# Kernel tuning notes

Measured on AMD Instinct MI355X. Metric: run time of the kernel, lower is better.

The kernel has to match this reference:

```python
import jax, jax.numpy as jnp
import numpy as np

N = 200000   # lane-graph nodes
C = 128      # n_map
S = 6        # num_scales
EP = 100000  # edges per pre/suc scale
EL = 25000   # left/right edges
EPS = 1e-5


def gn1(x, g, b):
    # GroupNorm(1, C) over shape [N, C]: normalize per node across channels, affine per channel
    mu = jnp.mean(x, axis=-1, keepdims=True)
    var = jnp.mean(jnp.square(x - mu), axis=-1, keepdims=True)
    return (x - mu) * jax.lax.rsqrt(var + EPS) * g + b


def setup_inputs() -> dict:
    key = jax.random.key(0)
    ks = jax.random.split(key, 32)
    f = lambda i, shape, s=1.0: jax.random.normal(ks[i], shape, dtype=jnp.float32) * s
    sc = 1.0 / np.sqrt(C)
    inp = {
        'control':   f(0, (N,)),
        'turn':      f(1, (N, 2)),
        'intersect': f(2, (N,)),
        'ctrs':      f(3, (N, 2)),
        'feats':     f(4, (N, 2)),
        'pre':   jax.random.randint(ks[5], (S, 2, EP), 0, N, dtype=jnp.int32),
        'suc':   jax.random.randint(ks[6], (S, 2, EP), 0, N, dtype=jnp.int32),
        'left':  jax.random.randint(ks[7], (2, EL), 0, N, dtype=jnp.int32),
        'right': jax.random.randint(ks[8], (2, EL), 0, N, dtype=jnp.int32),
        # input branch: Linear(2,C)+b, ReLU, Linear(C,C,no bias)+GroupNorm(1,C)
        'w_in1': f(9, (2, C), 0.7), 'b_in1': jnp.zeros((C,), jnp.float32),
        'w_in2': f(10, (C, C), sc), 'gn_in_g': jnp.ones((C,), jnp.float32), 'gn_in_b': jnp.zeros((C,), jnp.float32),
        # seg branch
        'w_seg1': f(11, (2, C), 0.7), 'b_seg1': jnp.zeros((C,), jnp.float32),
        'w_seg2': f(12, (C, C), sc), 'gn_seg_g': jnp.ones((C,), jnp.float32), 'gn_seg_b': jnp.zeros((C,), jnp.float32),
        # meta: Linear(C+4,C,no bias)+GN+ReLU
        'w_meta': f(13, (C + 4, C), sc), 'gn_meta_g': jnp.ones((C,), jnp.float32), 'gn_meta_b': jnp.zeros((C,), jnp.float32),
        # fuse dict, 4 layers
        'ctr_w':   f(14, (4, C, C), sc),
        'pre_w':   f(15, (4, S, C, C), sc),
        'suc_w':   f(16, (4, S, C, C), sc),
        'left_w':  f(17, (4, C, C), sc),
        'right_w': f(18, (4, C, C), sc),
        'norm_g': jnp.ones((4, C), jnp.float32), 'norm_b': jnp.zeros((4, C), jnp.float32),
        'ctr2_w': f(19, (4, C, C), sc),
        'ctr2_g': jnp.ones((4, C), jnp.float32), 'ctr2_b': jnp.zeros((4, C), jnp.float32),
    }
    return inp


def reference(control, turn, intersect, ctrs, feats, pre, suc, left, right,
              w_in1, b_in1, w_in2, gn_in_g, gn_in_b,
              w_seg1, b_seg1, w_seg2, gn_seg_g, gn_seg_b,
              w_meta, gn_meta_g, gn_meta_b,
              ctr_w, pre_w, suc_w, left_w, right_w,
              norm_g, norm_b, ctr2_w, ctr2_g, ctr2_b):
    # input / seg branches
    a = gn1(jax.nn.relu(ctrs @ w_in1 + b_in1) @ w_in2, gn_in_g, gn_in_b)
    b = gn1(jax.nn.relu(feats @ w_seg1 + b_seg1) @ w_seg2, gn_seg_g, gn_seg_b)
    feat = jax.nn.relu(a + b)
    # meta fuse
    meta = jnp.concatenate([feat, turn, control[:, None], intersect[:, None]], axis=1)
    feat = jax.nn.relu(gn1(meta @ w_meta, gn_meta_g, gn_meta_b))
    res = feat
    for i in range(4):
        temp = feat @ ctr_w[i]
        # multi-scale pre/suc: gather -> per-scale linear -> scatter-add
        pre_msg = jnp.einsum('sec,scd->sed', feat[pre[:, 1]], pre_w[i])   # [S,EP,C]
        temp = temp.at[pre[:, 0].reshape(-1)].add(pre_msg.reshape(-1, C))
        suc_msg = jnp.einsum('sec,scd->sed', feat[suc[:, 1]], suc_w[i])
        temp = temp.at[suc[:, 0].reshape(-1)].add(suc_msg.reshape(-1, C))
        temp = temp.at[left[0]].add(feat[left[1]] @ left_w[i])
        temp = temp.at[right[0]].add(feat[right[1]] @ right_w[i])
        feat = jax.nn.relu(gn1(temp, norm_g[i], norm_b[i]))
        feat = gn1(feat @ ctr2_w[i], ctr2_g[i], ctr2_b[i])
        feat = jax.nn.relu(feat + res)
        res = feat
    return (feat, ctrs)
```

## Files before the change

### kernel.cpp

```cpp
#include <hip/hip_runtime.h>

#define N_NODES 200000
#define CDIM 128
#define NSCALE 6
#define NEP 100000
#define NEL 25000
#define NCLS 14
#define NCHUNK 196

typedef unsigned short u16;
typedef unsigned int u32;

using fragAB = __attribute__((ext_vector_type(8))) short;
using fragC  = __attribute__((ext_vector_type(4))) float;

enum { P_PLAIN = 0, P_TWO = 1, P_META = 2 };
enum { E_GN = 1, E_RELU = 2 };

__device__ __forceinline__ float4 ld4(const float* p) { return *(const float4*)p; }

__device__ __forceinline__ u16 f2bf(float f) {
  u32 u = __builtin_bit_cast(u32, f);
  u = (u + 0x7fff + ((u >> 16) & 1)) >> 16;
  return (u16)u;
}
__device__ __forceinline__ u32 pk2(float a, float b) {
  return (u32)f2bf(a) | ((u32)f2bf(b) << 16);
}
__device__ __forceinline__ float bflo(u32 u) { return __builtin_bit_cast(float, u << 16); }
__device__ __forceinline__ float bfhi(u32 u) { return __builtin_bit_cast(float, u & 0xffff0000u); }

__device__ __forceinline__ void acc16(float* s, uint4 a, uint4 b) {
  s[0] += bflo(a.x); s[1] += bfhi(a.x); s[2]  += bflo(a.y); s[3]  += bfhi(a.y);
  s[4] += bflo(a.z); s[5] += bfhi(a.z); s[6]  += bflo(a.w); s[7]  += bfhi(a.w);
  s[8] += bflo(b.x); s[9] += bfhi(b.x); s[10] += bflo(b.y); s[11] += bfhi(b.y);
  s[12] += bflo(b.z); s[13] += bfhi(b.z); s[14] += bflo(b.w); s[15] += bfhi(b.w);
}

__host__ __device__ constexpr int idx_base(int c) {
  return (c < 12) ? c * NEP : 12 * NEP + (c - 12) * NEL;
}

__device__ __forceinline__ int wslot(int li, int c) {
  if (c < 0)  return 2 + li;
  if (c < 6)  return 18 + li * 6 + c;
  if (c < 12) return 42 + li * 6 + (c - 6);
  return (c == 12) ? (10 + li) : (14 + li);
}

template<int PRO, int EPI>
__global__ __launch_bounds__(256)
void mm_k(int M, int Kp,
          const float* __restrict__ Af, const float* __restrict__ A2f,
          const float* __restrict__ e0, const float* __restrict__ e1, const float* __restrict__ e2,
          const u16* __restrict__ Wt,
          float* __restrict__ Y, u16* __restrict__ Yb,
          const float* __restrict__ gn_g, const float* __restrict__ gn_b)
{
  constexpr int LSTR = 56;
  __shared__ u16 As[128 * LSTR];
  __shared__ u16 Bs[128 * LSTR];

  const int tid = threadIdx.x;
  const int lane = tid & 63, wid = tid >> 6;
  const int wm = (wid >> 1) * 64, wn = (wid & 1) * 64;
  const int q = lane >> 4, l16 = lane & 15;
  const int row0 = blockIdx.x * 128;
  const int srow = tid >> 1, shalf = tid & 1;

  fragC acc[4][4];
  #pragma unroll
  for (int i = 0; i < 4; i++)
    #pragma unroll
    for (int j = 0; j < 4; j++)
      #pragma unroll
      for (int e = 0; e < 4; e++) acc[i][j][e] = 0.0f;

  const int sgrow = row0 + srow;
  const bool svalid = (sgrow < M);
  float x0 = 0.f, x1 = 0.f, mx = 0.f, my = 0.f, mc = 0.f, mi = 0.f;
  if constexpr (PRO == P_TWO) {
    if (svalid) { x0 = Af[(size_t)sgrow * 2]; x1 = Af[(size_t)sgrow * 2 + 1]; }
  }
  if constexpr (PRO == P_META) {
    if (svalid) { mx = e0[(size_t)sgrow * 2]; my = e0[(size_t)sgrow * 2 + 1]; mc = e1[sgrow]; mi = e2[sgrow]; }
  }

  const int nk = Kp >> 5;
  for (int kt = 0; kt < nk; ++kt) {
    const int k0 = kt * 32 + shalf * 16;
    {
      u16* adst = &As[srow * LSTR + shalf * 16];
      float v[16];
      #pragma unroll
      for (int j = 0; j < 16; j++) v[j] = 0.f;
      if constexpr (PRO == P_TWO) {
        #pragma unroll
        for (int j0 = 0; j0 < 16; j0 += 4) {
          float4 wa = ld4(e0 + k0 + j0);
          float4 wb = ld4(e0 + 128 + k0 + j0);
          float4 bb = ld4(e1 + k0 + j0);
          v[j0]     = fmaxf(0.f, fmaf(x0, wa.x, fmaf(x1, wb.x, bb.x)));
          v[j0 + 1] = fmaxf(0.f, fmaf(x0, wa.y, fmaf(x1, wb.y, bb.y)));
          v[j0 + 2] = fmaxf(0.f, fmaf(x0, wa.z, fmaf(x1, wb.z, bb.z)));
          v[j0 + 3] = fmaxf(0.f, fmaf(x0, wa.w, fmaf(x1, wb.w, bb.w)));
        }
      } else {
        if (svalid) {
          if (k0 < 128) {
            const float* sa = Af + (size_t)sgrow * 128 + k0;
            const float* sb = A2f + (size_t)sgrow * 128 + k0;
            #pragma unroll
            for (int j0 = 0; j0 < 16; j0 += 4) {
              float4 a = ld4(sa + j0), b = ld4(sb + j0);
              v[j0]     = fmaxf(0.f, a.x + b.x);
              v[j0 + 1] = fmaxf(0.f, a.y + b.y);
              v[j0 + 2] = fmaxf(0.f, a.z + b.z);
              v[j0 + 3] = fmaxf(0.f, a.w + b.w);
            }
          } else {
            #pragma unroll
            for (int j = 0; j < 16; j++) {
              const int kk = k0 + j - 128;
              v[j] = (kk == 0) ? mx : (kk == 1) ? my : (kk == 2) ? mc : (kk == 3) ? mi : 0.f;
            }
          }
        }
      }
      u32 p[8];
      #pragma unroll
      for (int j = 0; j < 8; j++) p[j] = pk2(v[2 * j], v[2 * j + 1]);
      *(uint4*)adst = make_uint4(p[0], p[1], p[2], p[3]);
      *(uint4*)(adst + 8) = make_uint4(p[4], p[5], p[6], p[7]);
    }
    {
      const u16* s = Wt + (size_t)srow * Kp + k0;
      uint4 b0 = *(const uint4*)s, b1 = *(const uint4*)(s + 8);
      u16* bdst = &Bs[srow * LSTR + shalf * 16];
      *(uint4*)bdst = b0; *(uint4*)(bdst + 8) = b1;
    }
    __syncthreads();
    fragAB af[4], bf[4];
    #pragma unroll
    for (int t = 0; t < 4; t++) af[t] = *(const fragAB*)&As[(wm + t * 16 + l16) * LSTR + q * 8];
    #pragma unroll
    for (int t = 0; t < 4; t++) bf[t] = *(const fragAB*)&Bs[(wn + t * 16 + l16) * LSTR + q * 8];
    #pragma unroll
    for (int mt = 0; mt < 4; mt++)
      #pragma unroll
      for (int nt = 0; nt < 4; nt++)
        acc[mt][nt] = __builtin_amdgcn_mfma_f32_16x16x32_bf16(af[mt], bf[nt], acc[mt][nt], 0, 0, 0);
    __syncthreads();
  }

  __shared__ float2 red[128][2];
  __shared__ float2 stats[128];
  #pragma unroll
  for (int mt = 0; mt < 4; mt++)
    #pragma unroll
    for (int r = 0; r < 4; r++) {
      float s1 = acc[mt][0][r] + acc[mt][1][r] + acc[mt][2][r] + acc[mt][3][r];
      float s2 = acc[mt][0][r] * acc[mt][0][r] + acc[mt][1][r] * acc[mt][1][r]
               + acc[mt][2][r] * acc[mt][2][r] + acc[mt][3][r] * acc[mt][3][r];
      #pragma unroll
      for (int off = 1; off < 16; off <<= 1) {
        s1 += __shfl_xor(s1, off, 64);
        s2 += __shfl_xor(s2, off, 64);
      }
      if (l16 == 0) red[wm + mt * 16 + q * 4 + r][wid & 1] = make_float2(s1, s2);
    }
  __syncthreads();
  if (tid < 128) {
    const float2 p0 = red[tid][0], p1 = red[tid][1];
    const float m = (p0.x + p1.x) * (1.0f / 128.0f);
    const float var = (p0.y + p1.y) * (1.0f / 128.0f) - m * m;
    stats[tid] = make_float2(m, rsqrtf(var + 1e-5f));
  }
  __syncthreads();
  float gl[4], bl[4];
  #pragma unroll
  for (int nt = 0; nt < 4; nt++) {
    gl[nt] = gn_g[wn + nt * 16 + l16];
    bl[nt] = gn_b[wn + nt * 16 + l16];
  }
  #pragma unroll
  for (int mt = 0; mt < 4; mt++)
    #pragma unroll
    for (int r = 0; r < 4; r++) {
      const int rl = wm + mt * 16 + q * 4 + r;
      const int grow = row0 + rl;
      if (grow >= M) continue;
      const float2 st = stats[rl];
      #pragma unroll
      for (int nt = 0; nt < 4; nt++) {
        const int col = wn + nt * 16 + l16;
        float v = (acc[mt][nt][r] - st.x) * st.y * gl[nt] + bl[nt];
        if constexpr ((EPI & E_RELU) != 0) v = fmaxf(v, 0.f);
        if (Y)  Y[(size_t)grow * 128 + col] = v;
        if (Yb) Yb[(size_t)grow * 128 + col] = f2bf(v);
      }
    }
}

__global__ __launch_bounds__(256, 3)
void layer_k(const u16* __restrict__ Fin, u16* __restrict__ Fout,
             float* __restrict__ outf,
             const int* __restrict__ ptrs, const int* __restrict__ idxs,
             const u16* __restrict__ Wt, int li,
             const float* __restrict__ g1, const float* __restrict__ b1,
             const float* __restrict__ g2, const float* __restrict__ b2)
{
  constexpr int LSTR = 56, FSTR = 136;
  __shared__ u16 ldsA[128 * FSTR];
  __shared__ u16 Bs[128 * LSTR];
  __shared__ float2 red[128][2];
  __shared__ float2 stats[128];

  const int tid = threadIdx.x;
  const int lane = tid & 63, wid = tid >> 6;
  const int wm = (wid >> 1) * 64, wn = (wid & 1) * 64;
  const int q = lane >> 4, l16 = lane & 15;
  const int row0 = blockIdx.x * 128;
  const int srow = tid >> 1, shalf = tid & 1;
  const int sgrow = row0 + srow;
  const bool svalid = (sgrow < N_NODES);

  fragC acc[4][4];
  #pragma unroll
  for (int i = 0; i < 4; i++)
    #pragma unroll
    for (int j = 0; j < 4; j++)
      #pragma unroll
      for (int e = 0; e < 4; e++) acc[i][j][e] = 0.0f;

  for (int c = -1; c < NCLS; ++c) {
    const u16* W = Wt + (size_t)wslot(li, c) * 16384;

    if (c < 0) {
      uint4 a[8];
      #pragma unroll
      for (int j = 0; j < 8; j++) a[j] = make_uint4(0, 0, 0, 0);
      if (svalid) {
        const u16* s = Fin + (size_t)sgrow * 128 + shalf * 64;
        #pragma unroll
        for (int j = 0; j < 8; j++) a[j] = ((const uint4*)s)[j];
      }
      u16* adst = &ldsA[srow * FSTR + shalf * 64];
      #pragma unroll
      for (int j = 0; j < 8; j++) ((uint4*)adst)[j] = a[j];
    } else {
      int lo = 0, hi = 0;
      if (svalid) {
        const int* pc = ptrs + (size_t)c * (N_NODES + 1);
        hi = pc[sgrow]; lo = sgrow ? pc[sgrow - 1] : 0;
      }
      const int* ic = idxs + idx_base(c);
      #pragma unroll 1
      for (int hf = 0; hf < 2; ++hf) {
        const int off = shalf * 64 + hf * 32;
        float s[32];
        #pragma unroll
        for (int j = 0; j < 32; j++) s[j] = 0.f;
        int p = lo;
        for (; p + 2 <= hi; p += 2) {
          const u16* sp0 = Fin + (size_t)ic[p] * 128 + off;
          const u16* sp1 = Fin + (size_t)ic[p + 1] * 128 + off;
          uint4 a0 = ((const uint4*)sp0)[0], a1 = ((const uint4*)sp0)[1];
          uint4 a2 = ((const uint4*)sp0)[2], a3 = ((const uint4*)sp0)[3];
          uint4 b0 = ((const uint4*)sp1)[0], b1 = ((const uint4*)sp1)[1];
          uint4 b2 = ((const uint4*)sp1)[2], b3 = ((const uint4*)sp1)[3];
          acc16(s, a0, a1); acc16(s + 16, a2, a3);
          acc16(s, b0, b1); acc16(s + 16, b2, b3);
        }
        if (p < hi) {
          const u16* sp = Fin + (size_t)ic[p] * 128 + off;
          acc16(s, ((const uint4*)sp)[0], ((const uint4*)sp)[1]);
          acc16(s + 16, ((const uint4*)sp)[2], ((const uint4*)sp)[3]);
        }
        u32 pk[16];
        #pragma unroll
        for (int j = 0; j < 16; j++) pk[j] = pk2(s[2 * j], s[2 * j + 1]);
        u16* adst = &ldsA[srow * FSTR + off];
        ((uint4*)adst)[0] = make_uint4(pk[0],  pk[1],  pk[2],  pk[3]);
        ((uint4*)adst)[1] = make_uint4(pk[4],  pk[5],  pk[6],  pk[7]);
        ((uint4*)adst)[2] = make_uint4(pk[8],  pk[9],  pk[10], pk[11]);
        ((uint4*)adst)[3] = make_uint4(pk[12], pk[13], pk[14], pk[15]);
      }
    }

    uint4 pb0, pb1;
    {
      const u16* ws = W + (size_t)srow * 128 + shalf * 16;
      pb0 = *(const uint4*)ws; pb1 = *(const uint4*)(ws + 8);
    }
    __syncthreads();

    #pragma unroll
    for (int kt = 0; kt < 4; ++kt) {
      u16* bdst = &Bs[srow * LSTR + shalf * 16];
      *(uint4*)bdst = pb0; *(uint4*)(bdst + 8) = pb1;
      if (kt < 3) {
        const u16* ws = W + (size_t)srow * 128 + (kt + 1) * 32 + shalf * 16;
        pb0 = *(const uint4*)ws; pb1 = *(const uint4*)(ws + 8);
      }
      __syncthreads();
      fragAB af[4], bf[4];
      #pragma unroll
      for (int t = 0; t < 4; t++) af[t] = *(const fragAB*)&ldsA[(wm + t * 16 + l16) * FSTR + kt * 32 + q * 8];
      #pragma unroll
      for (int t = 0; t < 4; t++) bf[t] = *(const fragAB*)&Bs[(wn + t * 16 + l16) * LSTR + q * 8];
      #pragma unroll
      for (int mt = 0; mt < 4; mt++)
        #pragma unroll
        for (int nt = 0; nt < 4; nt++)
          acc[mt][nt] = __builtin_amdgcn_mfma_f32_16x16x32_bf16(af[mt], bf[nt], acc[mt][nt], 0, 0, 0);
      __syncthreads();
    }
  }

  #pragma unroll
  for (int mt = 0; mt < 4; mt++)
    #pragma unroll
    for (int r = 0; r < 4; r++) {
      float s1 = acc[mt][0][r] + acc[mt][1][r] + acc[mt][2][r] + acc[mt][3][r];
      float s2 = acc[mt][0][r] * acc[mt][0][r] + acc[mt][1][r] * acc[mt][1][r]
               + acc[mt][2][r] * acc[mt][2][r] + acc[mt][3][r] * acc[mt][3][r];
      #pragma unroll
      for (int off = 1; off < 16; off <<= 1) {
        s1 += __shfl_xor(s1, off, 64);
        s2 += __shfl_xor(s2, off, 64);
      }
      if (l16 == 0) red[wm + mt * 16 + q * 4 + r][wid & 1] = make_float2(s1, s2);
    }
  __syncthreads();
  if (tid < 128) {
    const float2 p0 = red[tid][0], p1 = red[tid][1];
    const float m = (p0.x + p1.x) * (1.0f / 128.0f);
    const float var = (p0.y + p1.y) * (1.0f / 128.0f) - m * m;
    stats[tid] = make_float2(m, rsqrtf(var + 1e-5f));
  }
  __syncthreads();
  {
    float gl[4], bl[4];
    #pragma unroll
    for (int nt = 0; nt < 4; nt++) {
      gl[nt] = g1[wn + nt * 16 + l16];
      bl[nt] = b1[wn + nt * 16 + l16];
    }
    #pragma unroll
    for (int mt = 0; mt < 4; mt++)
      #pragma unroll
      for (int r = 0; r < 4; r++) {
        const int rl = wm + mt * 16 + q * 4 + r;
        const float2 st = stats[rl];
        #pragma unroll
        for (int nt = 0; nt < 4; nt++) {
          const int col = wn + nt * 16 + l16;
          const float v = fmaxf(0.f, (acc[mt][nt][r] - st.x) * st.y * gl[nt] + bl[nt]);
          ldsA[rl * FSTR + col] = f2bf(v);
        }
      }
  }

  #pragma unroll
  for (int i = 0; i < 4; i++)
    #pragma unroll
    for (int j = 0; j < 4; j++)
      #pragma unroll
      for (int e = 0; e < 4; e++) acc[i][j][e] = 0.0f;
  {
    const u16* W2 = Wt + (size_t)(6 + li) * 16384;
    #pragma unroll
    for (int kt = 0; kt < 4; ++kt) {
      const int k0 = kt * 32 + shalf * 16;
      const u16* ws = W2 + (size_t)srow * 128 + k0;
      uint4 a = *(const uint4*)ws, b = *(const uint4*)(ws + 8);
      u16* bdst = &Bs[srow * LSTR + shalf * 16];
      *(uint4*)bdst = a; *(uint4*)(bdst + 8) = b;
      __syncthreads();
      fragAB af[4], bf[4];
      #pragma unroll
      for (int t = 0; t < 4; t++) af[t] = *(const fragAB*)&ldsA[(wm + t * 16 + l16) * FSTR + kt * 32 + q * 8];
      #pragma unroll
      for (int t = 0; t < 4; t++) bf[t] = *(const fragAB*)&Bs[(wn + t * 16 + l16) * LSTR + q * 8];
      #pragma unroll
      for (int mt = 0; mt < 4; mt++)
        #pragma unroll
        for (int nt = 0; nt < 4; nt++)
          acc[mt][nt] = __builtin_amdgcn_mfma_f32_16x16x32_bf16(af[mt], bf[nt], acc[mt][nt], 0, 0, 0);
      __syncthreads();
    }
  }

  #pragma unroll
  for (int mt = 0; mt < 4; mt++)
    #pragma unroll
    for (int r = 0; r < 4; r++) {
      float s1 = acc[mt][0][r] + acc[mt][1][r] + acc[mt][2][r] + acc[mt][3][r];
      float s2 = acc[mt][0][r] * acc[mt][0][r] + acc[mt][1][r] * acc[mt][1][r]
               + acc[mt][2][r] * acc[mt][2][r] + acc[mt][3][r] * acc[mt][3][r];
      #pragma unroll
      for (int off = 1; off < 16; off <<= 1) {
        s1 += __shfl_xor(s1, off, 64);
        s2 += __shfl_xor(s2, off, 64);
      }
      if (l16 == 0) red[wm + mt * 16 + q * 4 + r][wid & 1] = make_float2(s1, s2);
    }
  __syncthreads();
  if (tid < 128) {
    const float2 p0 = red[tid][0], p1 = red[tid][1];
    const float m = (p0.x + p1.x) * (1.0f / 128.0f);
    const float var = (p0.y + p1.y) * (1.0f / 128.0f) - m * m;
    stats[tid] = make_float2(m, rsqrtf(var + 1e-5f));
  }
  __syncthreads();
  {
    float gl[4], bl[4];
    #pragma unroll
    for (int nt = 0; nt < 4; nt++) {
      gl[nt] = g2[wn + nt * 16 + l16];
      bl[nt] = b2[wn + nt * 16 + l16];
    }
    #pragma unroll
    for (int mt = 0; mt < 4; mt++)
      #pragma unroll
      for (int r = 0; r < 4; r++) {
        const int rl = wm + mt * 16 + q * 4 + r;
        const int grow = row0 + rl;
        if (grow >= N_NODES) continue;
        const float2 st = stats[rl];
        #pragma unroll
        for (int nt = 0; nt < 4; nt++) {
          const int col = wn + nt * 16 + l16;
          const float res = bflo((u32)Fin[(size_t)grow * 128 + col]);
          float v = (acc[mt][nt][r] - st.x) * st.y * gl[nt] + bl[nt] + res;
          v = fmaxf(v, 0.f);
          if (outf) outf[(size_t)grow * 128 + col] = v;
          else      Fout[(size_t)grow * 128 + col] = f2bf(v);
        }
      }
  }
}

__global__ __launch_bounds__(256)
void prep_k(const float* __restrict__ in2, const float* __restrict__ seg2,
            const float* __restrict__ ctr, const float* __restrict__ ctr2,
            const float* __restrict__ lw, const float* __restrict__ rw,
            const float* __restrict__ pw, const float* __restrict__ sw,
            const float* __restrict__ meta, u16* __restrict__ Wt)
{
  const int id = blockIdx.x;
  const float* src;
  int K = 128, Kp = 128;
  if (id == 0) src = in2;
  else if (id == 1) src = seg2;
  else if (id < 6)  src = ctr  + (size_t)(id - 2) * 16384;
  else if (id < 10) src = ctr2 + (size_t)(id - 6) * 16384;
  else if (id < 14) src = lw   + (size_t)(id - 10) * 16384;
  else if (id < 18) src = rw   + (size_t)(id - 14) * 16384;
  else if (id < 42) src = pw   + (size_t)(id - 18) * 16384;
  else if (id < 66) src = sw   + (size_t)(id - 42) * 16384;
  else { src = meta; K = 132; Kp = 160; }
  u16* dst = Wt + (size_t)id * 16384;
  const int tot = 128 * Kp;
  for (int e = threadIdx.x; e < tot; e += 256) {
    const int n = e & 127, k = e >> 7;
    const float v = (k < K) ? src[(size_t)k * 128 + n] : 0.f;
    dst[(size_t)n * Kp + k] = f2bf(v);
  }
}

struct EdgeCfg { const int* dst[NCLS]; const int* src[NCLS]; int cnt[NCLS]; };

__global__ __launch_bounds__(256)
void hist_k(EdgeCfg cfg, int* __restrict__ ptrs)
{
  const int c = blockIdx.y;
  const int i = blockIdx.x * 256 + threadIdx.x;
  if (i < cfg.cnt[c]) atomicAdd(ptrs + (size_t)c * (N_NODES + 1) + cfg.dst[c][i], 1);
}

__global__ __launch_bounds__(256)
void scan1_k(const int* __restrict__ ptrs, int* __restrict__ part)
{
  const int c = blockIdx.y, b = blockIdx.x;
  const int* d = ptrs + (size_t)c * (N_NODES + 1) + b * 1024;
  const int rem = min(1024, N_NODES - b * 1024);
  int s = 0;
  for (int j = threadIdx.x; j < rem; j += 256) s += d[j];
  #pragma unroll
  for (int off = 32; off; off >>= 1) s += __shfl_xor(s, off, 64);
  __shared__ int r[4];
  if ((threadIdx.x & 63) == 0) r[threadIdx.x >> 6] = s;
  __syncthreads();
  if (threadIdx.x == 0) part[c * NCHUNK + b] = r[0] + r[1] + r[2] + r[3];
}

__global__ __launch_bounds__(64)
void scan2_k(int* __restrict__ part, int* __restrict__ ptrs)
{
  const int c = blockIdx.x;
  if (threadIdx.x) return;
  int* p = part + c * NCHUNK;
  int run = 0;
  for (int b = 0; b < NCHUNK; b++) { const int t = p[b]; p[b] = run; run += t; }
  ptrs[(size_t)c * (N_NODES + 1) + N_NODES] = run;
}

__global__ __launch_bounds__(256)
void scan3_k(int* __restrict__ ptrs, const int* __restrict__ part)
{
  const int c = blockIdx.y, b = blockIdx.x;
  int* d = ptrs + (size_t)c * (N_NODES + 1) + b * 1024;
  const int base = part[c * NCHUNK + b];
  const int gbase = b * 1024;
  const int i0 = threadIdx.x * 4;
  int v[4];
  #pragma unroll
  for (int j = 0; j < 4; j++) v[j] = (gbase + i0 + j < N_NODES) ? d[i0 + j] : 0;
  const int tsum = v[0] + v[1] + v[2] + v[3];
  __shared__ int sc[256];
  sc[threadIdx.x] = tsum;
  __syncthreads();
  #pragma unroll
  for (int off = 1; off < 256; off <<= 1) {
    const int t = (threadIdx.x >= off) ? sc[threadIdx.x - off] : 0;
    __syncthreads();
    sc[threadIdx.x] += t;
    __syncthreads();
  }
  int run = sc[threadIdx.x] - tsum + base;
  #pragma unroll
  for (int j = 0; j < 4; j++) {
    if (gbase + i0 + j < N_NODES) d[i0 + j] = run;
    run += v[j];
  }
}

__global__ __launch_bounds__(256)
void fill_k(EdgeCfg cfg, int* __restrict__ ptrs, int* __restrict__ idxs)
{
  const int c = blockIdx.y;
  const int i = blockIdx.x * 256 + threadIdx.x;
  if (i >= cfg.cnt[c]) return;
  const int d = cfg.dst[c][i];
  const int slot = atomicAdd(ptrs + (size_t)c * (N_NODES + 1) + d, 1);
  idxs[idx_base(c) + slot] = cfg.src[c][i];
}

__global__ __launch_bounds__(256)
void copy_k(const float* __restrict__ src, float* __restrict__ dst, int n)
{
  const int i = blockIdx.x * 256 + threadIdx.x;
  if (i < n) dst[i] = src[i];
}

extern "C" void kernel_launch(void* const* d_in, const int* in_sizes, int n_in,
                              void* d_out, int out_size, void* d_ws, size_t ws_size,
                              hipStream_t stream) {
  const float* control   = (const float*)d_in[0];
  const float* turn      = (const float*)d_in[1];
  const float* intersect = (const float*)d_in[2];
  const float* ctrs      = (const float*)d_in[3];
  const float* feats     = (const float*)d_in[4];
  const int*   pre   = (const int*)d_in[5];
  const int*   suc   = (const int*)d_in[6];
  const int*   left  = (const int*)d_in[7];
  const int*   right = (const int*)d_in[8];
  const float* w_in1   = (const float*)d_in[9];
  const float* b_in1   = (const float*)d_in[10];
  const float* w_in2   = (const float*)d_in[11];
  const float* gn_in_g = (const float*)d_in[12];
  const float* gn_in_b = (const float*)d_in[13];
  const float* w_seg1   = (const float*)d_in[14];
  const float* b_seg1   = (const float*)d_in[15];
  const float* w_seg2   = (const float*)d_in[16];
  const float* gn_seg_g = (const float*)d_in[17];
  const float* gn_seg_b = (const float*)d_in[18];
  const float* w_meta    = (const float*)d_in[19];
  const float* gn_meta_g = (const float*)d_in[20];
  const float* gn_meta_b = (const float*)d_in[21];
  const float* ctr_w   = (const float*)d_in[22];
  const float* pre_w   = (const float*)d_in[23];
  const float* suc_w   = (const float*)d_in[24];
  const float* left_w  = (const float*)d_in[25];
  const float* right_w = (const float*)d_in[26];
  const float* norm_g  = (const float*)d_in[27];
  const float* norm_b  = (const float*)d_in[28];
  const float* ctr2_w  = (const float*)d_in[29];
  const float* ctr2_g  = (const float*)d_in[30];
  const float* ctr2_b  = (const float*)d_in[31];

  const size_t NF = (size_t)N_NODES * CDIM;
  char* w = (char*)d_ws;
  float* Ta = (float*)w;  w += NF * 4;
  float* Tb = (float*)w;  w += NF * 4;
  u16* Fb0  = (u16*)w;    w += NF * 2;
  u16* Fb1  = (u16*)w;    w += NF * 2;
  u16* Wt   = (u16*)w;    w += (size_t)(67 * 16384 + 128 * 160) * 2;
  int* ptrs = (int*)w;    w += (size_t)NCLS * (N_NODES + 1) * 4;
  int* idxs = (int*)w;    w += (size_t)(12 * NEP + 2 * NEL) * 4;
  int* part = (int*)w;
  float* out = (float*)d_out;

  EdgeCfg cfg;
  for (int s = 0; s < NSCALE; s++) {
    cfg.dst[s] = pre + (size_t)s * 2 * NEP;     cfg.src[s] = pre + ((size_t)s * 2 + 1) * NEP;     cfg.cnt[s] = NEP;
    cfg.dst[6 + s] = suc + (size_t)s * 2 * NEP; cfg.src[6 + s] = suc + ((size_t)s * 2 + 1) * NEP; cfg.cnt[6 + s] = NEP;
  }
  cfg.dst[12] = left;  cfg.src[12] = left + NEL;  cfg.cnt[12] = NEL;
  cfg.dst[13] = right; cfg.src[13] = right + NEL; cfg.cnt[13] = NEL;

  const dim3 blk(256);
  const dim3 gN((N_NODES + 127) / 128);
  const dim3 gHist((NEP + 255) / 256, NCLS);
  const dim3 gScan(NCHUNK, NCLS);

  prep_k<<<dim3(67), blk, 0, stream>>>(w_in2, w_seg2, ctr_w, ctr2_w, left_w, right_w,
                                       pre_w, suc_w, w_meta, Wt);
  (void)hipMemsetAsync(ptrs, 0, (size_t)NCLS * (N_NODES + 1) * sizeof(int), stream);
  hist_k<<<gHist, blk, 0, stream>>>(cfg, ptrs);
  scan1_k<<<gScan, blk, 0, stream>>>(ptrs, part);
  scan2_k<<<dim3(NCLS), dim3(64), 0, stream>>>(part, ptrs);
  scan3_k<<<gScan, blk, 0, stream>>>(ptrs, part);
  fill_k<<<gHist, blk, 0, stream>>>(cfg, ptrs, idxs);

  mm_k<P_TWO, E_GN><<<gN, blk, 0, stream>>>(N_NODES, 128, ctrs, nullptr,
      w_in1, b_in1, nullptr, Wt + 0 * 16384, Ta, nullptr, gn_in_g, gn_in_b);
  mm_k<P_TWO, E_GN><<<gN, blk, 0, stream>>>(N_NODES, 128, feats, nullptr,
      w_seg1, b_seg1, nullptr, Wt + 1 * 16384, Tb, nullptr, gn_seg_g, gn_seg_b);
  mm_k<P_META, E_GN | E_RELU><<<gN, blk, 0, stream>>>(N_NODES, 160, Ta, Tb,
      turn, control, intersect, Wt + 66 * 16384, nullptr, Fb0, gn_meta_g, gn_meta_b);

  for (int i = 0; i < 4; i++) {
    const u16* Fin = (i & 1) ? Fb1 : Fb0;
    u16* Fout      = (i & 1) ? Fb0 : Fb1;
    layer_k<<<gN, blk, 0, stream>>>(Fin, Fout, (i == 3) ? out : nullptr,
        ptrs, idxs, Wt, i,
        norm_g + i * 128, norm_b + i * 128, ctr2_g + i * 128, ctr2_b + i * 128);
  }

  copy_k<<<dim3((2 * N_NODES + 255) / 256), blk, 0, stream>>>(ctrs, out + NF, 2 * N_NODES);
}
```

Before: 2.068 ms.

## Load MFMA weight fragments directly from global, drop B staging in LDS

Removes the shared-memory B tile: weight fragments for every GEMM are now read straight from global (L2-resident) memory into MFMA registers. The first ctr GEMM also reads the A operand directly from Fin instead of staging it in LDS. This cuts LDS use and most per-k-tile barriers, and raises launch bounds to 4 blocks per CU. It also drops the 2-way unroll of the gather loop. The cost is more global or L2 load traffic and latency on the MFMA inner loop, plus tighter register pressure.

```diff
diff --git a/kernel.cpp b/kernel.cpp
--- a/kernel.cpp
+++ b/kernel.cpp
@@ -202,7 +202,7 @@
     }
 }
 
-__global__ __launch_bounds__(256, 3)
+__global__ __launch_bounds__(256, 4)
 void layer_k(const u16* __restrict__ Fin, u16* __restrict__ Fout,
              float* __restrict__ outf,
              const int* __restrict__ ptrs, const int* __restrict__ idxs,
@@ -210,9 +210,8 @@
              const float* __restrict__ g1, const float* __restrict__ b1,
              const float* __restrict__ g2, const float* __restrict__ b2)
 {
-  constexpr int LSTR = 56, FSTR = 136;
+  constexpr int FSTR = 136;
   __shared__ u16 ldsA[128 * FSTR];
-  __shared__ u16 Bs[128 * LSTR];
   __shared__ float2 red[128][2];
   __shared__ float2 stats[128];
 
@@ -233,88 +232,77 @@
       #pragma unroll
       for (int e = 0; e < 4; e++) acc[i][j][e] = 0.0f;
 
-  for (int c = -1; c < NCLS; ++c) {
-    const u16* W = Wt + (size_t)wslot(li, c) * 16384;
-
-    if (c < 0) {
-      uint4 a[8];
-      #pragma unroll
-      for (int j = 0; j < 8; j++) a[j] = make_uint4(0, 0, 0, 0);
-      if (svalid) {
-        const u16* s = Fin + (size_t)sgrow * 128 + shalf * 64;
-        #pragma unroll
-        for (int j = 0; j < 8; j++) a[j] = ((const uint4*)s)[j];
-      }
-      u16* adst = &ldsA[srow * FSTR + shalf * 64];
-      #pragma unroll
-      for (int j = 0; j < 8; j++) ((uint4*)adst)[j] = a[j];
-    } else {
-      int lo = 0, hi = 0;
-      if (svalid) {
-        const int* pc = ptrs + (size_t)c * (N_NODES + 1);
-        hi = pc[sgrow]; lo = sgrow ? pc[sgrow - 1] : 0;
-      }
-      const int* ic = idxs + idx_base(c);
-      #pragma unroll 1
-      for (int hf = 0; hf < 2; ++hf) {
-        const int off = shalf * 64 + hf * 32;
-        float s[32];
-        #pragma unroll
-        for (int j = 0; j < 32; j++) s[j] = 0.f;
-        int p = lo;
-        for (; p + 2 <= hi; p += 2) {
-          const u16* sp0 = Fin + (size_t)ic[p] * 128 + off;
-          const u16* sp1 = Fin + (size_t)ic[p + 1] * 128 + off;
-          uint4 a0 = ((const uint4*)sp0)[0], a1 = ((const uint4*)sp0)[1];
-          uint4 a2 = ((const uint4*)sp0)[2], a3 = ((const uint4*)sp0)[3];
-          uint4 b0 = ((const uint4*)sp1)[0], b1 = ((const uint4*)sp1)[1];
-          uint4 b2 = ((const uint4*)sp1)[2], b3 = ((const uint4*)sp1)[3];
-          acc16(s, a0, a1); acc16(s + 16, a2, a3);
-          acc16(s, b0, b1); acc16(s + 16, b2, b3);
-        }
-        if (p < hi) {
-          const u16* sp = Fin + (size_t)ic[p] * 128 + off;
-          acc16(s, ((const uint4*)sp)[0], ((const uint4*)sp)[1]);
-          acc16(s + 16, ((const uint4*)sp)[2], ((const uint4*)sp)[3]);
-        }
-        u32 pk[16];
-        #pragma unroll
-        for (int j = 0; j < 16; j++) pk[j] = pk2(s[2 * j], s[2 * j + 1]);
-        u16* adst = &ldsA[srow * FSTR + off];
-        ((uint4*)adst)[0] = make_uint4(pk[0],  pk[1],  pk[2],  pk[3]);
-        ((uint4*)adst)[1] = make_uint4(pk[4],  pk[5],  pk[6],  pk[7]);
-        ((uint4*)adst)[2] = make_uint4(pk[8],  pk[9],  pk[10], pk[11]);
-        ((uint4*)adst)[3] = make_uint4(pk[12], pk[13], pk[14], pk[15]);
-      }
-    }
-
-    uint4 pb0, pb1;
-    {
-      const u16* ws = W + (size_t)srow * 128 + shalf * 16;
-      pb0 = *(const uint4*)ws; pb1 = *(const uint4*)(ws + 8);
-    }
-    __syncthreads();
-
+  {
+    const u16* W = Wt + (size_t)(2 + li) * 16384;
     #pragma unroll
     for (int kt = 0; kt < 4; ++kt) {
-      u16* bdst = &Bs[srow * LSTR + shalf * 16];
-      *(uint4*)bdst = pb0; *(uint4*)(bdst + 8) = pb1;
-      if (kt < 3) {
-        const u16* ws = W + (size_t)srow * 128 + (kt + 1) * 32 + shalf * 16;
-        pb0 = *(const uint4*)ws; pb1 = *(const uint4*)(ws + 8);
-      }
-      __syncthreads();
       fragAB af[4], bf[4];
       #pragma unroll
-      for (int t = 0; t < 4; t++) af[t] = *(const fragAB*)&ldsA[(wm + t * 16 + l16) * FSTR + kt * 32 + q * 8];
-      #pragma unroll
-      for (int t = 0; t < 4; t++) bf[t] = *(const fragAB*)&Bs[(wn + t * 16 + l16) * LSTR + q * 8];
+      for (int t = 0; t < 4; t++) {
+        int r = row0 + wm + t * 16 + l16;
+        r = (r < N_NODES) ? r : (N_NODES - 1);
+        af[t] = *(const fragAB*)(Fin + (size_t)r * 128 + kt * 32 + q * 8);
+      }
+      #pragma unroll
+      for (int t = 0; t < 4; t++)
+        bf[t] = *(const fragAB*)(W + (size_t)(wn + t * 16 + l16) * 128 + kt * 32 + q * 8);
       #pragma unroll
       for (int mt = 0; mt < 4; mt++)
         #pragma unroll
         for (int nt = 0; nt < 4; nt++)
           acc[mt][nt] = __builtin_amdgcn_mfma_f32_16x16x32_bf16(af[mt], bf[nt], acc[mt][nt], 0, 0, 0);
-      __syncthreads();
+    }
+  }
+
+  for (int c = 0; c < NCLS; ++c) {
+    const u16* W = Wt + (size_t)wslot(li, c) * 16384;
+    int lo = 0, hi = 0;
+    if (svalid) {
+      const int* pc = ptrs + (size_t)c * (N_NODES + 1);
+      hi = pc[sgrow]; lo = sgrow ? pc[sgrow - 1] : 0;
+    }
+    const int* ic = idxs + idx_base(c);
+
+    __syncthreads();
+
+    #pragma unroll 1
+    for (int hf = 0; hf < 2; ++hf) {
+      const int off = shalf * 64 + hf * 32;
+      float s[32];
+      #pragma unroll
+      for (int j = 0; j < 32; j++) s[j] = 0.f;
+      for (int p = lo; p < hi; ++p) {
+        const u16* sp = Fin + (size_t)ic[p] * 128 + off;
+        uint4 a0 = ((const uint4*)sp)[0], a1 = ((const uint4*)sp)[1];
+        uint4 a2 = ((const uint4*)sp)[2], a3 = ((const uint4*)sp)[3];
+        acc16(s, a0, a1); acc16(s + 16, a2, a3);
+      }
+      u32 pk[16];
+      #pragma unroll
+      for (int j = 0; j < 16; j++) pk[j] = pk2(s[2 * j], s[2 * j + 1]);
+      u16* adst = &ldsA[srow * FSTR + off];
+      ((uint4*)adst)[0] = make_uint4(pk[0],  pk[1],  pk[2],  pk[3]);
+      ((uint4*)adst)[1] = make_uint4(pk[4],  pk[5],  pk[6],  pk[7]);
+      ((uint4*)adst)[2] = make_uint4(pk[8],  pk[9],  pk[10], pk[11]);
+      ((uint4*)adst)[3] = make_uint4(pk[12], pk[13], pk[14], pk[15]);
+    }
+
+    __syncthreads();
+
+    #pragma unroll
+    for (int kt = 0; kt < 4; ++kt) {
+      fragAB af[4], bf[4];
+      #pragma unroll
+      for (int t = 0; t < 4; t++)
+        af[t] = *(const fragAB*)&ldsA[(wm + t * 16 + l16) * FSTR + kt * 32 + q * 8];
+      #pragma unroll
+      for (int t = 0; t < 4; t++)
+        bf[t] = *(const fragAB*)(W + (size_t)(wn + t * 16 + l16) * 128 + kt * 32 + q * 8);
+      #pragma unroll
+      for (int mt = 0; mt < 4; mt++)
+        #pragma unroll
+        for (int nt = 0; nt < 4; nt++)
+          acc[mt][nt] = __builtin_amdgcn_mfma_f32_16x16x32_bf16(af[mt], bf[nt], acc[mt][nt], 0, 0, 0);
     }
   }
 
@@ -368,27 +356,23 @@
     for (int j = 0; j < 4; j++)
       #pragma unroll
       for (int e = 0; e < 4; e++) acc[i][j][e] = 0.0f;
+  __syncthreads();
   {
     const u16* W2 = Wt + (size_t)(6 + li) * 16384;
     #pragma unroll
     for (int kt = 0; kt < 4; ++kt) {
-      const int k0 = kt * 32 + shalf * 16;
-      const u16* ws = W2 + (size_t)srow * 128 + k0;
-      uint4 a = *(const uint4*)ws, b = *(const uint4*)(ws + 8);
-      u16* bdst = &Bs[srow * LSTR + shalf * 16];
-      *(uint4*)bdst = a; *(uint4*)(bdst + 8) = b;
-      __syncthreads();
       fragAB af[4], bf[4];
       #pragma unroll
-      for (int t = 0; t < 4; t++) af[t] = *(const fragAB*)&ldsA[(wm + t * 16 + l16) * FSTR + kt * 32 + q * 8];
-      #pragma unroll
-      for (int t = 0; t < 4; t++) bf[t] = *(const fragAB*)&Bs[(wn + t * 16 + l16) * LSTR + q * 8];
+      for (int t = 0; t < 4; t++)
+        af[t] = *(const fragAB*)&ldsA[(wm + t * 16 + l16) * FSTR + kt * 32 + q * 8];
+      #pragma unroll
+      for (int t = 0; t < 4; t++)
+        bf[t] = *(const fragAB*)(W2 + (size_t)(wn + t * 16 + l16) * 128 + kt * 32 + q * 8);
       #pragma unroll
       for (int mt = 0; mt < 4; mt++)
         #pragma unroll
         for (int nt = 0; nt < 4; nt++)
           acc[mt][nt] = __builtin_amdgcn_mfma_f32_16x16x32_bf16(af[mt], bf[nt], acc[mt][nt], 0, 0, 0);
-      __syncthreads();
     }
   }
 
```

Measured after the change: 2.429 ms. +17.4%, slower.
